# Optimization experiments

Measured on AMD Instinct MI355X. Metric: run time of the kernel, lower is better.

## Reference

```python
import jax, jax.numpy as jnp
import numpy as np

DIM = 768
N_HEADS = 12
HEAD_DIM = DIM // N_HEADS
B, S = 16, 1024


def setup_inputs() -> dict:
    key = jax.random.key(0)
    k1, k2, k3, k4, k5 = jax.random.split(key, 5)
    scale = 0.02
    return {
        "x": jax.random.normal(k1, (B, S, DIM), dtype=jnp.float32),
        "W_attn": jax.random.normal(k2, (DIM, 3 * DIM), dtype=jnp.float32) * scale,
        "b_attn": jnp.zeros((3 * DIM,), dtype=jnp.float32),
        "W_proj": jax.random.normal(k3, (DIM, DIM), dtype=jnp.float32) * scale,
        "b_proj": jnp.zeros((DIM,), dtype=jnp.float32),
    }


def reference(x, W_attn, b_attn, W_proj, b_proj):
    # Dropout layers act as identity (eval mode) for a deterministic reference.
    Bsz, Sq, D = x.shape
    qkv = x @ W_attn + b_attn                      # [B, S, 3D]
    q, k, v = jnp.split(qkv, 3, axis=-1)
    q = q.reshape(Bsz, Sq, N_HEADS, HEAD_DIM)
    k = k.reshape(Bsz, Sq, N_HEADS, HEAD_DIM)
    v = v.reshape(Bsz, Sq, N_HEADS, HEAD_DIM)
    # scores: [B, H, S, S]
    w = jnp.einsum('bqhd,bkhd->bhqk', q, k) / jnp.sqrt(jnp.float32(HEAD_DIM))
    causal = jnp.tril(jnp.ones((Sq, Sq), dtype=bool))
    mask_value = jnp.finfo(w.dtype).min
    w = jnp.where(causal[None, None], w, mask_value)
    w = jax.nn.softmax(w, axis=-1)
    attn = jnp.einsum('bhqk,bkhd->bqhd', w, v).reshape(Bsz, Sq, D)
    return attn @ W_proj + b_proj
```

## Files before the change

### kernel.cpp

```cpp
#include <hip/hip_runtime.h>
#include <hip/hip_bf16.h>
#include <math.h>

#define BDIM 16
#define SEQ 1024
#define DIM 768
#define NH 12
#define HD 64
#define M_ROWS (BDIM * SEQ)
#define N_QKV (3 * DIM)
#define QN (BDIM * NH * SEQ * HD)

typedef __attribute__((ext_vector_type(8))) short bf16x8_t;
typedef __attribute__((ext_vector_type(4))) float f32x4_t;
typedef __attribute__((ext_vector_type(16))) float f32x16_t;
typedef __attribute__((ext_vector_type(4))) unsigned int u32x4_t;

__device__ __forceinline__ unsigned short f2bf(float x) {
    return __builtin_bit_cast(unsigned short, __float2bfloat16(x));
}

__device__ __forceinline__ void gld_lds16(const void* g, void* l) {
    __builtin_amdgcn_global_load_lds(
        (const __attribute__((address_space(1))) void*)g,
        (__attribute__((address_space(3))) void*)l, 16, 0, 0);
}

__device__ __forceinline__ unsigned int cvt_pk_bf16(float a, float b) {
    unsigned int r;
    asm("v_cvt_pk_bf16_f32 %0, %1, %2" : "=v"(r) : "v"(a), "v"(b));
    return r;
}

__device__ __forceinline__ void perm32swap(unsigned int& a, unsigned int& b) {
    asm("v_permlane32_swap_b32 %0, %1" : "+v"(a), "+v"(b));
}

__device__ __forceinline__ float exp2_fast(float x) {
    float r;
    asm("v_exp_f32 %0, %1" : "=v"(r) : "v"(x));
    return r;
}

__device__ __forceinline__ int xcd_remap(int lin, int chunk) {
    return (lin & 7) * chunk + (lin >> 3);
}

#define QSCALE 0.18033688011112042f

#define X_BLOCKS 6144
#define WA_TILES 432
#define WP_TILES 144

__global__ __launch_bounds__(256) void prep(
    const float* __restrict__ x, const float* __restrict__ Wa,
    const float* __restrict__ Wp,
    unsigned short* __restrict__ xb, unsigned short* __restrict__ Wat,
    unsigned short* __restrict__ Wpt)
{
    __shared__ unsigned short T[64][72];
    const int bid = blockIdx.x;
    const int tid = threadIdx.x;

    if (bid < X_BLOCKS) {
        size_t base = (size_t)bid * 2048 + tid * 8;
        float4 f0 = *(const float4*)&x[base];
        float4 f1 = *(const float4*)&x[base + 4];
        unsigned short tmp[8] = {f2bf(f0.x), f2bf(f0.y), f2bf(f0.z), f2bf(f0.w),
                                 f2bf(f1.x), f2bf(f1.y), f2bf(f1.z), f2bf(f1.w)};
        *(uint4*)&xb[base] = *(uint4*)tmp;
        return;
    }
    const float* W; unsigned short* Wt; int N, kt, nt;
    int b2 = bid - X_BLOCKS;
    if (b2 < WA_TILES) { W = Wa; Wt = Wat; N = N_QKV; kt = b2 / 36; nt = b2 % 36; }
    else { b2 -= WA_TILES; W = Wp; Wt = Wpt; N = DIM; kt = b2 / 12; nt = b2 % 12; }
    const int k0 = kt * 64, n0 = nt * 64;
#pragma unroll
    for (int c = 0; c < 4; c++) {
        int idx = c * 256 + tid;
        int r = idx >> 4;
        int c4 = (idx & 15) * 4;
        float4 v = *(const float4*)&W[(size_t)(k0 + r) * N + n0 + c4];
        T[r][c4 + 0] = f2bf(v.x);
        T[r][c4 + 1] = f2bf(v.y);
        T[r][c4 + 2] = f2bf(v.z);
        T[r][c4 + 3] = f2bf(v.w);
    }
    __syncthreads();
#pragma unroll
    for (int c = 0; c < 2; c++) {
        int idx = c * 256 + tid;
        int n = idx >> 3;
        int ch = (idx & 7) * 8;
        unsigned short tmp[8];
#pragma unroll
        for (int j = 0; j < 8; j++) tmp[j] = T[ch + j][n];
        *(uint4*)&Wt[(size_t)(n0 + n) * DIM + k0 + ch] = *(uint4*)tmp;
    }
}

__device__ __forceinline__ void stage_tile256(
    const unsigned short* __restrict__ Ab, const unsigned short* __restrict__ Bt,
    int bm, int bn, int k0, unsigned short* Asd, unsigned short* Bsd, int tid)
{
#pragma unroll
    for (int rr = 0; rr < 4; rr++) {
        int idx = rr * 512 + tid;
        int r = idx >> 3;
        int gch = (idx & 7) ^ (r & 7);
        gld_lds16(&Ab[(size_t)(bm + r) * DIM + k0 + gch * 8], &Asd[idx * 8]);
    }
#pragma unroll
    for (int rr = 0; rr < 4; rr++) {
        int idx = rr * 512 + tid;
        int r = idx >> 3;
        int gch = (idx & 7) ^ (r & 7);
        gld_lds16(&Bt[(size_t)(bn + r) * DIM + k0 + gch * 8], &Bsd[idx * 8]);
    }
}

__global__ __launch_bounds__(512, 1) void gemm_qkv_mfma(
    const unsigned short* __restrict__ Ab,
    const unsigned short* __restrict__ Bt,
    const float* __restrict__ bias,
    unsigned short* __restrict__ Qo, unsigned short* __restrict__ Ko,
    unsigned short* __restrict__ Vt)
{
    __shared__ unsigned short As[2 * 16384];
    __shared__ unsigned short Bs[2 * 16384];

    const int tid = threadIdx.x;
    const int lane = tid & 63;
    const int w = tid >> 6;
    const int wm = w >> 2, wn = w & 3;
    const int ln = lane & 15, quad = lane >> 4;

    const int lin = blockIdx.x + 9 * blockIdx.y;
    const int jj = xcd_remap(lin, 72);
    const int bm = (jj / 9) * 256, bn = (jj % 9) * 256;

    f32x4_t acc[8][4];
#pragma unroll
    for (int i = 0; i < 8; i++)
#pragma unroll
        for (int j = 0; j < 4; j++) acc[i][j] = (f32x4_t){0.f, 0.f, 0.f, 0.f};

    stage_tile256(Ab, Bt, bm, bn, 0, As, Bs, tid);
    stage_tile256(Ab, Bt, bm, bn, 64, As + 16384, Bs + 16384, tid);
    asm volatile("s_waitcnt vmcnt(8)" ::: "memory");
    __builtin_amdgcn_sched_barrier(0);
    __builtin_amdgcn_s_barrier();
    __builtin_amdgcn_sched_barrier(0);

    for (int k = 0; k < 12; k++) {
        const unsigned short* As_ = As + (k & 1) * 16384;
        const unsigned short* Bs_ = Bs + (k & 1) * 16384;

        bf16x8_t bfr[4][2];
#pragma unroll
        for (int nt = 0; nt < 4; nt++)
#pragma unroll
            for (int kk = 0; kk < 2; kk++) {
                int r = wn * 64 + nt * 16 + ln;
                int c = (kk * 4 + quad) ^ (ln & 7);
                bfr[nt][kk] = *(const bf16x8_t*)&Bs_[r * 64 + c * 8];
            }
#pragma unroll
        for (int q = 0; q < 4; q++) {
            bf16x8_t af[2][2];
#pragma unroll
            for (int mi = 0; mi < 2; mi++)
#pragma unroll
                for (int kk = 0; kk < 2; kk++) {
                    int r = wm * 128 + (q * 2 + mi) * 16 + ln;
                    int c = (kk * 4 + quad) ^ (ln & 7);
                    af[mi][kk] = *(const bf16x8_t*)&As_[r * 64 + c * 8];
                }
            __builtin_amdgcn_s_setprio(1);
#pragma unroll
            for (int mi = 0; mi < 2; mi++)
#pragma unroll
                for (int nt = 0; nt < 4; nt++)
#pragma unroll
                    for (int kk = 0; kk < 2; kk++)
                        acc[q * 2 + mi][nt] = __builtin_amdgcn_mfma_f32_16x16x32_bf16(
                            af[mi][kk], bfr[nt][kk], acc[q * 2 + mi][nt], 0, 0, 0);
            __builtin_amdgcn_s_setprio(0);
        }

        if (k < 11) {
            __builtin_amdgcn_s_barrier();
            __builtin_amdgcn_sched_barrier(0);
            if (k < 10) {
                stage_tile256(Ab, Bt, bm, bn, (k + 2) * 64,
                              As + (k & 1) * 16384, Bs + (k & 1) * 16384, tid);
                asm volatile("s_waitcnt vmcnt(8)" ::: "memory");
            } else {
                asm volatile("s_waitcnt vmcnt(0)" ::: "memory");
            }
            __builtin_amdgcn_sched_barrier(0);
            __builtin_amdgcn_s_barrier();
            __builtin_amdgcn_sched_barrier(0);
        }
    }
    __syncthreads();

    const int nb = bn + wn * 64;
    const int part = nb / DIM;
    const int h = (nb % DIM) >> 6;
    const float scale = (part == 0) ? QSCALE : 1.0f;
    const int mb = bm + wm * 128;
    const int b_ = mb >> 10;
    const int s0 = mb & 1023;
    unsigned short* Wb = (w < 4) ? (As + w * 4608) : (Bs + (w - 4) * 4608);

    float bias_v[4];
#pragma unroll
    for (int nt = 0; nt < 4; nt++) bias_v[nt] = bias[nb + nt * 16 + ln];

#pragma unroll
    for (int g = 0; g < 2; g++) {
        if (part < 2) {
#pragma unroll
            for (int lt = 0; lt < 4; lt++)
#pragma unroll
                for (int nt = 0; nt < 4; nt++)
#pragma unroll
                    for (int r = 0; r < 4; r++)
                        Wb[(lt * 16 + quad * 4 + r) * 72 + nt * 16 + ln] =
                            f2bf((acc[g * 4 + lt][nt][r] + bias_v[nt]) * scale);
            unsigned short* dst = (part == 0) ? Qo : Ko;
            size_t obase = (((size_t)b_ * NH + h) * SEQ + s0 + g * 64) * HD;
#pragma unroll
            for (int c = 0; c < 8; c++) {
                int idx = c * 64 + lane;
                int rr = idx >> 3;
                int ch = (idx & 7) * 8;
                *(uint4*)&dst[obase + (size_t)rr * HD + ch] = *(uint4*)&Wb[rr * 72 + ch];
            }
        } else {
#pragma unroll
            for (int lt = 0; lt < 4; lt++)
#pragma unroll
                for (int nt = 0; nt < 4; nt++)
#pragma unroll
                    for (int r = 0; r < 4; r++)
                        Wb[(nt * 16 + ln) * 72 + lt * 16 + quad * 4 + r] =
                            f2bf(acc[g * 4 + lt][nt][r] + bias_v[nt]);
            size_t obase = ((size_t)b_ * NH + h) * (size_t)HD * SEQ;
#pragma unroll
            for (int c = 0; c < 8; c++) {
                int idx = c * 64 + lane;
                int d = idx >> 3;
                int ch = (idx & 7) * 8;
                *(uint4*)&Vt[obase + (size_t)d * SEQ + s0 + g * 64 + ch] =
                    *(uint4*)&Wb[d * 72 + ch];
            }
        }
    }
}

__global__ __launch_bounds__(512, 1) void gemm_proj_mfma(
    const unsigned short* __restrict__ Ab,
    const unsigned short* __restrict__ Bt,
    const float* __restrict__ bias,
    float* __restrict__ C)
{
    __shared__ unsigned short As[2 * 16384];
    __shared__ unsigned short Bs[2 * 16384];

    const int tid = threadIdx.x;
    const int lane = tid & 63;
    const int w = tid >> 6;
    const int wm = w >> 2, wn = w & 3;
    const int ln = lane & 15, quad = lane >> 4;

    const int lin = blockIdx.x + 3 * blockIdx.y;
    const int jj = xcd_remap(lin, 24);
    const int bm = (jj / 3) * 256, bn = (jj % 3) * 256;

    f32x4_t acc[8][4];
#pragma unroll
    for (int i = 0; i < 8; i++)
#pragma unroll
        for (int j = 0; j < 4; j++) acc[i][j] = (f32x4_t){0.f, 0.f, 0.f, 0.f};

    stage_tile256(Ab, Bt, bm, bn, 0, As, Bs, tid);
    stage_tile256(Ab, Bt, bm, bn, 64, As + 16384, Bs + 16384, tid);
    asm volatile("s_waitcnt vmcnt(8)" ::: "memory");
    __builtin_amdgcn_sched_barrier(0);
    __builtin_amdgcn_s_barrier();
    __builtin_amdgcn_sched_barrier(0);

    for (int k = 0; k < 12; k++) {
        const unsigned short* As_ = As + (k & 1) * 16384;
        const unsigned short* Bs_ = Bs + (k & 1) * 16384;

        bf16x8_t bfr[4][2];
#pragma unroll
        for (int nt = 0; nt < 4; nt++)
#pragma unroll
            for (int kk = 0; kk < 2; kk++) {
                int r = wn * 64 + nt * 16 + ln;
                int c = (kk * 4 + quad) ^ (ln & 7);
                bfr[nt][kk] = *(const bf16x8_t*)&Bs_[r * 64 + c * 8];
            }
#pragma unroll
        for (int q = 0; q < 4; q++) {
            bf16x8_t af[2][2];
#pragma unroll
            for (int mi = 0; mi < 2; mi++)
#pragma unroll
                for (int kk = 0; kk < 2; kk++) {
                    int r = wm * 128 + (q * 2 + mi) * 16 + ln;
                    int c = (kk * 4 + quad) ^ (ln & 7);
                    af[mi][kk] = *(const bf16x8_t*)&As_[r * 64 + c * 8];
                }
            __builtin_amdgcn_s_setprio(1);
#pragma unroll
            for (int mi = 0; mi < 2; mi++)
#pragma unroll
                for (int nt = 0; nt < 4; nt++)
#pragma unroll
                    for (int kk = 0; kk < 2; kk++)
                        acc[q * 2 + mi][nt] = __builtin_amdgcn_mfma_f32_16x16x32_bf16(
                            af[mi][kk], bfr[nt][kk], acc[q * 2 + mi][nt], 0, 0, 0);
            __builtin_amdgcn_s_setprio(0);
        }

        if (k < 11) {
            __builtin_amdgcn_s_barrier();
            __builtin_amdgcn_sched_barrier(0);
            if (k < 10) {
                stage_tile256(Ab, Bt, bm, bn, (k + 2) * 64,
                              As + (k & 1) * 16384, Bs + (k & 1) * 16384, tid);
                asm volatile("s_waitcnt vmcnt(8)" ::: "memory");
            } else {
                asm volatile("s_waitcnt vmcnt(0)" ::: "memory");
            }
            __builtin_amdgcn_sched_barrier(0);
            __builtin_amdgcn_s_barrier();
            __builtin_amdgcn_sched_barrier(0);
        }
    }

    const int nb = bn + wn * 64;
    float bias_v[4];
#pragma unroll
    for (int nt = 0; nt < 4; nt++) bias_v[nt] = bias[nb + nt * 16 + ln];
#pragma unroll
    for (int mt = 0; mt < 8; mt++)
#pragma unroll
        for (int nt = 0; nt < 4; nt++)
#pragma unroll
            for (int r = 0; r < 4; r++) {
                int m = bm + wm * 128 + mt * 16 + quad * 4 + r;
                C[(size_t)m * DIM + nb + nt * 16 + ln] = acc[mt][nt][r] + bias_v[nt];
            }
}

#define SWZ(r) ((((r) & 7)) ^ ((((r) >> 3)) & 3))

__global__ __launch_bounds__(256, 3) void attn_mfma(
    const unsigned short* __restrict__ Qg, const unsigned short* __restrict__ Kg,
    const unsigned short* __restrict__ Vt, unsigned short* __restrict__ Out)
{
    __shared__ unsigned short Ks[2][4096];
    __shared__ unsigned short Vs[2][4096];

    const int tid = threadIdx.x;
    const int lane = tid & 63;
    const int w = tid >> 6;
    const int wpair = w >> 1;
    const int whigh = w & 1;
    const int l31 = lane & 31;
    const int hi = lane >> 5;
    const int l7 = lane & 7;
    const int sw3 = (l31 >> 3) & 3;

    const int lin = blockIdx.x + 4 * blockIdx.y;
    const int jj = xcd_remap(lin, 96);
    const int bxn = jj & 3;
    const int bh = jj >> 2;
    const size_t gbase = (size_t)bh * SEQ * HD;
    const int b_ = bh / NH;
    const int h = bh % NH;

    bf16x8_t vones;
#pragma unroll
    for (int i = 0; i < 8; i++) vones[i] = (short)0x3F80;

    for (int ph = 0; ph < 2; ph++) {
        const int qt = ph ? bxn : 7 - bxn;
        const int qbase = qt * 128;
        const int ntiles = 2 * qt + 2;
        const int wtiles = 2 * qt + 1 + wpair;
        const int qr0 = qbase + w * 32;

        bf16x8_t aq[4];
#pragma unroll
        for (int ds = 0; ds < 4; ds++)
            aq[ds] = *(const bf16x8_t*)
                &Qg[gbase + (size_t)(qr0 + l31) * HD + ds * 16 + hi * 8];

        f32x16_t acc[2];
        f32x16_t lacc;
#pragma unroll
        for (int j = 0; j < 16; j++) {
            acc[0][j] = 0.f; acc[1][j] = 0.f; lacc[j] = 0.f;
        }

        __syncthreads();

#pragma unroll
        for (int i = 0; i < 2; i++) {
            int idx = i * 256 + tid;
            int r = idx >> 3;
            int gc = (idx & 7) ^ SWZ(r);
            gld_lds16(&Kg[gbase + (size_t)r * HD + gc * 8], &Ks[0][idx * 8]);
            gld_lds16(&Vt[gbase + (size_t)r * SEQ + gc * 8], &Vs[0][idx * 8]);
        }

        for (int t = 0; t < ntiles; t++) {
            __syncthreads();
            const int cur = t & 1;

            if (t + 1 < ntiles) {
                const int nk0 = (t + 1) * 64;
#pragma unroll
                for (int i = 0; i < 2; i++) {
                    int idx = i * 256 + tid;
                    int r = idx >> 3;
                    int gc = (idx & 7) ^ SWZ(r);
                    gld_lds16(&Kg[gbase + (size_t)(nk0 + r) * HD + gc * 8],
                              &Ks[cur ^ 1][idx * 8]);
                    gld_lds16(&Vt[gbase + (size_t)r * SEQ + nk0 + gc * 8],
                              &Vs[cur ^ 1][idx * 8]);
                }
            }
            if (t >= wtiles) continue;
            const bool diag = (t == 2 * qt + wpair);
            const int kgend = diag ? (1 + whigh) : 2;

            for (int kg = 0; kg < kgend; kg++) {
                bf16x8_t kf[4];
#pragma unroll
                for (int ds = 0; ds < 4; ds++)
                    kf[ds] = *(const bf16x8_t*)
                        &Ks[cur][(kg * 32 + l31) * 64 +
                                 (((ds * 2 + hi) ^ l7 ^ sw3) * 8)];

                f32x16_t sa;
#pragma unroll
                for (int j = 0; j < 16; j++) sa[j] = 0.f;
                __builtin_amdgcn_s_setprio(1);
#pragma unroll
                for (int ds = 0; ds < 4; ds++)
                    sa = __builtin_amdgcn_mfma_f32_32x32x16_bf16(
                        kf[ds], aq[ds], sa, 0, 0, 0);
                __builtin_amdgcn_s_setprio(0);

                const bool dm = diag && (kg == whigh);
                const int qr = qr0 + l31;
                float p[16];
#pragma unroll
                for (int j = 0; j < 16; j++) {
                    float pv = exp2_fast(sa[j]);
                    if (dm) {
                        int key = t * 64 + kg * 32 + (j & 3) + 8 * (j >> 2) + 4 * hi;
                        if (key > qr) pv = 0.f;
                    }
                    p[j] = pv;
                }
                unsigned int c0 = cvt_pk_bf16(p[0], p[1]);
                unsigned int c1 = cvt_pk_bf16(p[2], p[3]);
                unsigned int c2 = cvt_pk_bf16(p[4], p[5]);
                unsigned int c3 = cvt_pk_bf16(p[6], p[7]);
                unsigned int c4 = cvt_pk_bf16(p[8], p[9]);
                unsigned int c5 = cvt_pk_bf16(p[10], p[11]);
                unsigned int c6 = cvt_pk_bf16(p[12], p[13]);
                unsigned int c7 = cvt_pk_bf16(p[14], p[15]);
                perm32swap(c0, c2);
                perm32swap(c1, c3);
                perm32swap(c4, c6);
                perm32swap(c5, c7);
                u32x4_t u0, u1;
                u0[0] = c0; u0[1] = c1; u0[2] = c2; u0[3] = c3;
                u1[0] = c4; u1[1] = c5; u1[2] = c6; u1[3] = c7;
                bf16x8_t pa0 = __builtin_bit_cast(bf16x8_t, u0);
                bf16x8_t pa1 = __builtin_bit_cast(bf16x8_t, u1);

                __builtin_amdgcn_s_setprio(1);
                lacc = __builtin_amdgcn_mfma_f32_32x32x16_bf16(
                    pa0, vones, lacc, 0, 0, 0);
                lacc = __builtin_amdgcn_mfma_f32_32x32x16_bf16(
                    pa1, vones, lacc, 0, 0, 0);
#pragma unroll
                for (int dh = 0; dh < 2; dh++) {
                    bf16x8_t vf0 = *(const bf16x8_t*)
                        &Vs[cur][(dh * 32 + l31) * 64 +
                                 (((kg * 4 + 0 + hi) ^ l7 ^ sw3) * 8)];
                    acc[dh] = __builtin_amdgcn_mfma_f32_32x32x16_bf16(
                        pa0, vf0, acc[dh], 0, 0, 0);
                    bf16x8_t vf1 = *(const bf16x8_t*)
                        &Vs[cur][(dh * 32 + l31) * 64 +
                                 (((kg * 4 + 2 + hi) ^ l7 ^ sw3) * 8)];
                    acc[dh] = __builtin_amdgcn_mfma_f32_32x32x16_bf16(
                        pa1, vf1, acc[dh], 0, 0, 0);
                }
                __builtin_amdgcn_s_setprio(0);
            }
        }

        float rin[16];
#pragma unroll
        for (int j = 0; j < 16; j++) rin[j] = 1.0f / lacc[j];
#pragma unroll
        for (int dh = 0; dh < 2; dh++)
#pragma unroll
            for (int j = 0; j < 16; j++) {
                int row = qr0 + (j & 3) + 8 * (j >> 2) + 4 * hi;
                Out[((size_t)b_ * SEQ + row) * DIM + h * HD + dh * 32 + l31] =
                    f2bf(acc[dh][j] * rin[j]);
            }
    }
}

extern "C" void kernel_launch(void* const* d_in, const int* in_sizes, int n_in,
                              void* d_out, int out_size, void* d_ws, size_t ws_size,
                              hipStream_t stream) {
    const float* x  = (const float*)d_in[0];
    const float* Wa = (const float*)d_in[1];
    const float* ba = (const float*)d_in[2];
    const float* Wp = (const float*)d_in[3];
    const float* bp = (const float*)d_in[4];
    float* out = (float*)d_out;

    unsigned short* ws = (unsigned short*)d_ws;
    unsigned short* Qg  = ws;
    unsigned short* Kg  = Qg + (size_t)QN;
    unsigned short* Vt  = Kg + (size_t)QN;
    unsigned short* xb  = Vt + (size_t)QN;
    unsigned short* AO  = xb;
    unsigned short* Wat = xb + (size_t)QN;
    unsigned short* Wpt = Wat + (size_t)(N_QKV * DIM);

    prep<<<X_BLOCKS + WA_TILES + WP_TILES, 256, 0, stream>>>(
        x, Wa, Wp, xb, Wat, Wpt);

    dim3 g_qkv(N_QKV / 256, M_ROWS / 256);
    gemm_qkv_mfma<<<g_qkv, 512, 0, stream>>>(xb, Wat, ba, Qg, Kg, Vt);

    dim3 g_attn(4, BDIM * NH);
    attn_mfma<<<g_attn, 256, 0, stream>>>(Qg, Kg, Vt, AO);

    dim3 g_proj(DIM / 256, M_ROWS / 256);
    gemm_proj_mfma<<<g_proj, 512, 0, stream>>>(AO, Wpt, bp, out);
}
```

Before: 258.3 us.

## Interleave next-tile global-to-LDS loads with MFMA phases in both GEMMs

Both GEMM kernels change their prefetch schedule. Instead of loading tile k+2 after the compute loop, tile k+1 is now loaded into the other buffer during the q-phases of the current tile: A is issued in phase 0 and B in phase 1. The goal is to spread the global loads across the compute and get more of their latency hidden behind MFMA work. In exchange the prefetch distance drops from two tiles to one, and every q-phase gains two workgroup barriers, which could add stalls.

```diff
diff --git a/kernel.cpp b/kernel.cpp
--- a/kernel.cpp
+++ b/kernel.cpp
@@ -100,23 +100,16 @@
     }
 }
 
-__device__ __forceinline__ void stage_tile256(
-    const unsigned short* __restrict__ Ab, const unsigned short* __restrict__ Bt,
-    int bm, int bn, int k0, unsigned short* Asd, unsigned short* Bsd, int tid)
+__device__ __forceinline__ void stage_half256(
+    const unsigned short* __restrict__ srcRow0, int k0,
+    unsigned short* lbuf, int half, int tid)
 {
 #pragma unroll
-    for (int rr = 0; rr < 4; rr++) {
-        int idx = rr * 512 + tid;
+    for (int c = 0; c < 2; c++) {
+        int idx = half * 1024 + c * 512 + tid;
         int r = idx >> 3;
         int gch = (idx & 7) ^ (r & 7);
-        gld_lds16(&Ab[(size_t)(bm + r) * DIM + k0 + gch * 8], &Asd[idx * 8]);
-    }
-#pragma unroll
-    for (int rr = 0; rr < 4; rr++) {
-        int idx = rr * 512 + tid;
-        int r = idx >> 3;
-        int gch = (idx & 7) ^ (r & 7);
-        gld_lds16(&Bt[(size_t)(bn + r) * DIM + k0 + gch * 8], &Bsd[idx * 8]);
+        gld_lds16(&srcRow0[(size_t)r * DIM + k0 + gch * 8], &lbuf[idx * 8]);
     }
 }
 
@@ -139,6 +132,8 @@
     const int lin = blockIdx.x + 9 * blockIdx.y;
     const int jj = xcd_remap(lin, 72);
     const int bm = (jj / 9) * 256, bn = (jj % 9) * 256;
+    const unsigned short* Arow = Ab + (size_t)bm * DIM;
+    const unsigned short* Brow = Bt + (size_t)bn * DIM;
 
     f32x4_t acc[8][4];
 #pragma unroll
@@ -146,9 +141,11 @@
 #pragma unroll
         for (int j = 0; j < 4; j++) acc[i][j] = (f32x4_t){0.f, 0.f, 0.f, 0.f};
 
-    stage_tile256(Ab, Bt, bm, bn, 0, As, Bs, tid);
-    stage_tile256(Ab, Bt, bm, bn, 64, As + 16384, Bs + 16384, tid);
-    asm volatile("s_waitcnt vmcnt(8)" ::: "memory");
+    stage_half256(Arow, 0, As, 0, tid);
+    stage_half256(Arow, 0, As, 1, tid);
+    stage_half256(Brow, 0, Bs, 0, tid);
+    stage_half256(Brow, 0, Bs, 1, tid);
+    asm volatile("s_waitcnt vmcnt(0)" ::: "memory");
     __builtin_amdgcn_sched_barrier(0);
     __builtin_amdgcn_s_barrier();
     __builtin_amdgcn_sched_barrier(0);
@@ -156,18 +153,23 @@
     for (int k = 0; k < 12; k++) {
         const unsigned short* As_ = As + (k & 1) * 16384;
         const unsigned short* Bs_ = Bs + (k & 1) * 16384;
+        unsigned short* Asn = As + ((k & 1) ^ 1) * 16384;
+        unsigned short* Bsn = Bs + ((k & 1) ^ 1) * 16384;
+        const int k1 = (k + 1) * 64;
 
         bf16x8_t bfr[4][2];
 #pragma unroll
-        for (int nt = 0; nt < 4; nt++)
-#pragma unroll
-            for (int kk = 0; kk < 2; kk++) {
-                int r = wn * 64 + nt * 16 + ln;
-                int c = (kk * 4 + quad) ^ (ln & 7);
-                bfr[nt][kk] = *(const bf16x8_t*)&Bs_[r * 64 + c * 8];
-            }
-#pragma unroll
         for (int q = 0; q < 4; q++) {
+            if (q == 0) {
+#pragma unroll
+                for (int nt = 0; nt < 4; nt++)
+#pragma unroll
+                    for (int kk = 0; kk < 2; kk++) {
+                        int r = wn * 64 + nt * 16 + ln;
+                        int c = (kk * 4 + quad) ^ (ln & 7);
+                        bfr[nt][kk] = *(const bf16x8_t*)&Bs_[r * 64 + c * 8];
+                    }
+            }
             bf16x8_t af[2][2];
 #pragma unroll
             for (int mi = 0; mi < 2; mi++)
@@ -177,6 +179,18 @@
                     int c = (kk * 4 + quad) ^ (ln & 7);
                     af[mi][kk] = *(const bf16x8_t*)&As_[r * 64 + c * 8];
                 }
+            if (k < 11) {
+                if (q == 0) {
+                    stage_half256(Arow, k1, Asn, 0, tid);
+                    stage_half256(Arow, k1, Asn, 1, tid);
+                } else if (q == 1) {
+                    stage_half256(Brow, k1, Bsn, 0, tid);
+                    stage_half256(Brow, k1, Bsn, 1, tid);
+                }
+            }
+            __builtin_amdgcn_s_barrier();
+            asm volatile("s_waitcnt lgkmcnt(0)" ::: "memory");
+            __builtin_amdgcn_sched_barrier(0);
             __builtin_amdgcn_s_setprio(1);
 #pragma unroll
             for (int mi = 0; mi < 2; mi++)
@@ -187,18 +201,11 @@
                         acc[q * 2 + mi][nt] = __builtin_amdgcn_mfma_f32_16x16x32_bf16(
                             af[mi][kk], bfr[nt][kk], acc[q * 2 + mi][nt], 0, 0, 0);
             __builtin_amdgcn_s_setprio(0);
+            __builtin_amdgcn_s_barrier();
         }
 
         if (k < 11) {
-            __builtin_amdgcn_s_barrier();
-            __builtin_amdgcn_sched_barrier(0);
-            if (k < 10) {
-                stage_tile256(Ab, Bt, bm, bn, (k + 2) * 64,
-                              As + (k & 1) * 16384, Bs + (k & 1) * 16384, tid);
-                asm volatile("s_waitcnt vmcnt(8)" ::: "memory");
-            } else {
-                asm volatile("s_waitcnt vmcnt(0)" ::: "memory");
-            }
+            asm volatile("s_waitcnt vmcnt(0)" ::: "memory");
             __builtin_amdgcn_sched_barrier(0);
             __builtin_amdgcn_s_barrier();
             __builtin_amdgcn_sched_barrier(0);
@@ -279,6 +286,8 @@
     const int lin = blockIdx.x + 3 * blockIdx.y;
     const int jj = xcd_remap(lin, 24);
     const int bm = (jj / 3) * 256, bn = (jj % 3) * 256;
+    const unsigned short* Arow = Ab + (size_t)bm * DIM;
+    const unsigned short* Brow = Bt + (size_t)bn * DIM;
 
     f32x4_t acc[8][4];
 #pragma unroll
@@ -286,9 +295,11 @@
 #pragma unroll
         for (int j = 0; j < 4; j++) acc[i][j] = (f32x4_t){0.f, 0.f, 0.f, 0.f};
 
-    stage_tile256(Ab, Bt, bm, bn, 0, As, Bs, tid);
-    stage_tile256(Ab, Bt, bm, bn, 64, As + 16384, Bs + 16384, tid);
-    asm volatile("s_waitcnt vmcnt(8)" ::: "memory");
+    stage_half256(Arow, 0, As, 0, tid);
+    stage_half256(Arow, 0, As, 1, tid);
+    stage_half256(Brow, 0, Bs, 0, tid);
+    stage_half256(Brow, 0, Bs, 1, tid);
+    asm volatile("s_waitcnt vmcnt(0)" ::: "memory");
     __builtin_amdgcn_sched_barrier(0);
     __builtin_amdgcn_s_barrier();
     __builtin_amdgcn_sched_barrier(0);
@@ -296,18 +307,23 @@
     for (int k = 0; k < 12; k++) {
         const unsigned short* As_ = As + (k & 1) * 16384;
         const unsigned short* Bs_ = Bs + (k & 1) * 16384;
+        unsigned short* Asn = As + ((k & 1) ^ 1) * 16384;
+        unsigned short* Bsn = Bs + ((k & 1) ^ 1) * 16384;
+        const int k1 = (k + 1) * 64;
 
         bf16x8_t bfr[4][2];
 #pragma unroll
-        for (int nt = 0; nt < 4; nt++)
-#pragma unroll
-            for (int kk = 0; kk < 2; kk++) {
-                int r = wn * 64 + nt * 16 + ln;
-                int c = (kk * 4 + quad) ^ (ln & 7);
-                bfr[nt][kk] = *(const bf16x8_t*)&Bs_[r * 64 + c * 8];
-            }
-#pragma unroll
         for (int q = 0; q < 4; q++) {
+            if (q == 0) {
+#pragma unroll
+                for (int nt = 0; nt < 4; nt++)
+#pragma unroll
+                    for (int kk = 0; kk < 2; kk++) {
+                        int r = wn * 64 + nt * 16 + ln;
+                        int c = (kk * 4 + quad) ^ (ln & 7);
+                        bfr[nt][kk] = *(const bf16x8_t*)&Bs_[r * 64 + c * 8];
+                    }
+            }
             bf16x8_t af[2][2];
 #pragma unroll
             for (int mi = 0; mi < 2; mi++)
@@ -317,6 +333,18 @@
                     int c = (kk * 4 + quad) ^ (ln & 7);
                     af[mi][kk] = *(const bf16x8_t*)&As_[r * 64 + c * 8];
                 }
+            if (k < 11) {
+                if (q == 0) {
+                    stage_half256(Arow, k1, Asn, 0, tid);
+                    stage_half256(Arow, k1, Asn, 1, tid);
+                } else if (q == 1) {
+                    stage_half256(Brow, k1, Bsn, 0, tid);
+                    stage_half256(Brow, k1, Bsn, 1, tid);
+                }
+            }
+            __builtin_amdgcn_s_barrier();
+            asm volatile("s_waitcnt lgkmcnt(0)" ::: "memory");
+            __builtin_amdgcn_sched_barrier(0);
             __builtin_amdgcn_s_setprio(1);
 #pragma unroll
             for (int mi = 0; mi < 2; mi++)
@@ -327,18 +355,11 @@
                         acc[q * 2 + mi][nt] = __builtin_amdgcn_mfma_f32_16x16x32_bf16(
                             af[mi][kk], bfr[nt][kk], acc[q * 2 + mi][nt], 0, 0, 0);
             __builtin_amdgcn_s_setprio(0);
+            __builtin_amdgcn_s_barrier();
         }
 
         if (k < 11) {
-            __builtin_amdgcn_s_barrier();
-            __builtin_amdgcn_sched_barrier(0);
-            if (k < 10) {
-                stage_tile256(Ab, Bt, bm, bn, (k + 2) * 64,
-                              As + (k & 1) * 16384, Bs + (k & 1) * 16384, tid);
-                asm volatile("s_waitcnt vmcnt(8)" ::: "memory");
-            } else {
-                asm volatile("s_waitcnt vmcnt(0)" ::: "memory");
-            }
+            asm volatile("s_waitcnt vmcnt(0)" ::: "memory");
             __builtin_amdgcn_sched_barrier(0);
             __builtin_amdgcn_s_barrier();
             __builtin_amdgcn_sched_barrier(0);
```

After: 258.4 us. Within noise of the previous version (+0.1%).
